# Kernel tuning notes

Measured on AMD Instinct MI355X. Metric: run time of the kernel, lower is better.

## Reference

```python
import jax, jax.numpy as jnp
import numpy as np

B, F = 2_000_000, 21
NUM_CLASSES = 7
RANGE_MIN, RANGE_MAX = 0.0, 1000.0  # normal_ranges[k] == (0, 1000) for all k


def setup_inputs() -> dict:
    key = jax.random.key(0)
    k1, k2, k3, k4 = jax.random.split(key, 4)
    inputs = jax.random.normal(k1, (B, F), dtype=jnp.float32) * 100.0
    # targets: integer sensor readings; column 2 must be a class value in {100,...,700}
    targets = jax.random.randint(k2, (B, F), -200, 1200, dtype=jnp.int32)
    cls_col = jax.random.randint(k3, (B,), 1, NUM_CLASSES + 1, dtype=jnp.int32) * 100
    targets = targets.at[:, 2].set(cls_col)
    weights = jax.random.uniform(k4, (NUM_CLASSES,), dtype=jnp.float32, minval=0.5, maxval=1.5)
    return {"inputs": inputs, "targets": targets, "weights": weights}


def reference(inputs, targets, weights):
    # class_to_index {100:0,...,700:6} == value // 100 - 1 (pure arithmetic, no host lookup)
    mapped = targets[:, 2] // 100 - 1                      # [B] int
    sample_w = weights[mapped]                              # [B]
    diff = inputs - targets.astype(inputs.dtype)            # [B, F]
    weighted_loss = jnp.mean(sample_w[:, None] * diff * diff, axis=1)  # [B]
    # range penalty on sensor value targets[:, 1] vs normal range (0, 1000)
    v = targets[:, 1].astype(inputs.dtype)                  # [B]
    below = jnp.square(v - RANGE_MIN)
    above = jnp.square(v - RANGE_MAX)
    pen = jnp.where(v < RANGE_MIN, below, jnp.where(v > RANGE_MAX, above, 0.0))
    penalty = jnp.sum(pen)                                  # scalar
    return jnp.mean(weighted_loss + penalty)
```

## Files before the change

kernel.cpp:

```cpp
#include <hip/hip_runtime.h>


#define TOTAL_ELEMS 42000000
#define NVEC (TOTAL_ELEMS / 4)
#define NBLK 2048
#define NTHR 256

__device__ __forceinline__ void accum4(int v, const float* __restrict__ x,
                                       const int* __restrict__ t, const float* ws,
                                       float& amain, float& apen)
{
    const int idx0 = v << 2;
    const float4 xf = reinterpret_cast<const float4*>(x)[v];
    const int4   ti = reinterpret_cast<const int4*>(t)[v];
    const int rowA = idx0 / 21;
    const int colA = idx0 - rowA * 21;
    const int rowB = (idx0 + 3) / 21;
    const float wA = ws[t[rowA * 21 + 2] / 100 - 1];
    const float wB = ws[t[rowB * 21 + 2] / 100 - 1];
    const float xs[4] = {xf.x, xf.y, xf.z, xf.w};
    const int   tv[4] = {ti.x, ti.y, ti.z, ti.w};
    #pragma unroll
    for (int j = 0; j < 4; ++j) {
        const int col   = colA + j;
        const float wj  = (col < 21) ? wA : wB;
        const int  ccol = (col < 21) ? col : col - 21;
        const float tf  = (float)tv[j];
        const float d   = xs[j] - tf;
        amain = fmaf(wj * d, d, amain);
        if (ccol == 1) {
            apen += tf < 0.f ? tf * tf
                  : (tf > 1000.f ? (tf - 1000.f) * (tf - 1000.f) : 0.f);
        }
    }
}

__global__ __launch_bounds__(NTHR) void wmse_main(
    const float* __restrict__ x, const int* __restrict__ t,
    const float* __restrict__ w, float* __restrict__ part)
{
    __shared__ float ws[8];
    if (threadIdx.x < 7) ws[threadIdx.x] = w[threadIdx.x];
    __syncthreads();

    float am0 = 0.f, am1 = 0.f, ap0 = 0.f, ap1 = 0.f;
    const int stride = NBLK * NTHR;
    for (int v = blockIdx.x * NTHR + threadIdx.x; v < NVEC; v += 2 * stride) {
        accum4(v, x, t, ws, am0, ap0);
        if (v + stride < NVEC) accum4(v + stride, x, t, ws, am1, ap1);
    }
    float amain = am0 + am1, apen = ap0 + ap1;

    #pragma unroll
    for (int off = 32; off > 0; off >>= 1) {
        amain += __shfl_down(amain, off);
        apen  += __shfl_down(apen,  off);
    }
    __shared__ float rm[4], rp[4];
    const int wid = threadIdx.x >> 6;
    if ((threadIdx.x & 63) == 0) { rm[wid] = amain; rp[wid] = apen; }
    __syncthreads();
    if (threadIdx.x == 0) {
        part[2 * blockIdx.x]     = rm[0] + rm[1] + rm[2] + rm[3];
        part[2 * blockIdx.x + 1] = rp[0] + rp[1] + rp[2] + rp[3];
    }
}

__global__ __launch_bounds__(256) void wmse_reduce(
    const float* __restrict__ part, float* __restrict__ out)
{
    float m = 0.f, p = 0.f;
    for (int i = threadIdx.x; i < NBLK; i += 256) {
        m += part[2 * i];
        p += part[2 * i + 1];
    }
    #pragma unroll
    for (int off = 32; off > 0; off >>= 1) {
        m += __shfl_down(m, off);
        p += __shfl_down(p, off);
    }
    __shared__ float rm[4], rp[4];
    const int wid = threadIdx.x >> 6;
    if ((threadIdx.x & 63) == 0) { rm[wid] = m; rp[wid] = p; }
    __syncthreads();
    if (threadIdx.x == 0) {
        out[0] = (rm[0] + rm[1] + rm[2] + rm[3]) * (1.0f / 42000000.0f)
               + (rp[0] + rp[1] + rp[2] + rp[3]);
    }
}

extern "C" void kernel_launch(void* const* d_in, const int* in_sizes, int n_in,
                              void* d_out, int out_size, void* d_ws, size_t ws_size,
                              hipStream_t stream)
{
    const float* x = (const float*)d_in[0];
    const int*   t = (const int*)d_in[1];
    const float* w = (const float*)d_in[2];
    float* part = (float*)d_ws;
    wmse_main<<<NBLK, NTHR, 0, stream>>>(x, t, w, part);
    wmse_reduce<<<1, 256, 0, stream>>>(part, (float*)d_out);
}
```

Baseline: 339.4 us.

## Software-pipeline loads with double-buffered chunk registers and branchless per-vector compute

Splits each float4/int4 chunk into a load phase and a compute phase, then runs a fully scheduled loop that keeps eight chunks in flight across two register buffers so memory latency overlaps arithmetic. It also halves the grid to 1024 blocks with a fixed trip count and replaces the per-element branchy weight and penalty logic with branchless selects and a clamp. The cost is higher register pressure and hardcoded sizing that only fits this exact element count (40*T plus a tail).

```diff
diff --git a/kernel.cpp b/kernel.cpp
--- a/kernel.cpp
+++ b/kernel.cpp
@@ -1,41 +1,48 @@
 #include <hip/hip_runtime.h>
 
 
-#define TOTAL_ELEMS 42000000
-#define NVEC (TOTAL_ELEMS / 4)
-#define NBLK 2048
+#define NVEC 10500000
+#define NBLK 1024
 #define NTHR 256
+#define T    (NBLK * NTHR)
 
-__device__ __forceinline__ void accum4(int v, const float* __restrict__ x,
-                                       const int* __restrict__ t, const float* ws,
-                                       float& amain, float& apen)
+struct CH { float4 xf; int4 ti; int tcA, tcB, colA; };
+
+__device__ __forceinline__ void ch_load(int v, const float* __restrict__ x,
+                                        const int* __restrict__ t, CH& c)
 {
     const int idx0 = v << 2;
-    const float4 xf = reinterpret_cast<const float4*>(x)[v];
-    const int4   ti = reinterpret_cast<const int4*>(t)[v];
+    c.xf = reinterpret_cast<const float4*>(x)[v];
+    c.ti = reinterpret_cast<const int4*>(t)[v];
     const int rowA = idx0 / 21;
-    const int colA = idx0 - rowA * 21;
+    c.colA = idx0 - rowA * 21;
     const int rowB = (idx0 + 3) / 21;
-    const float wA = ws[t[rowA * 21 + 2] / 100 - 1];
-    const float wB = ws[t[rowB * 21 + 2] / 100 - 1];
-    const float xs[4] = {xf.x, xf.y, xf.z, xf.w};
-    const int   tv[4] = {ti.x, ti.y, ti.z, ti.w};
-    #pragma unroll
-    for (int j = 0; j < 4; ++j) {
-        const int col   = colA + j;
-        const float wj  = (col < 21) ? wA : wB;
-        const int  ccol = (col < 21) ? col : col - 21;
-        const float tf  = (float)tv[j];
-        const float d   = xs[j] - tf;
-        amain = fmaf(wj * d, d, amain);
-        if (ccol == 1) {
-            apen += tf < 0.f ? tf * tf
-                  : (tf > 1000.f ? (tf - 1000.f) * (tf - 1000.f) : 0.f);
-        }
-    }
+    c.tcA = t[rowA * 21 + 2];
+    c.tcB = t[rowB * 21 + 2];
 }
 
-__global__ __launch_bounds__(NTHR) void wmse_main(
+__device__ __forceinline__ void ch_compute(const CH& c, const float* ws,
+                                           float& am, float& ap)
+{
+    const float wA = ws[c.tcA / 100 - 1];
+    const float wB = ws[c.tcB / 100 - 1];
+    const float tf0 = (float)c.ti.x, tf1 = (float)c.ti.y,
+                tf2 = (float)c.ti.z, tf3 = (float)c.ti.w;
+    const float d0 = c.xf.x - tf0, d1 = c.xf.y - tf1,
+                d2 = c.xf.z - tf2, d3 = c.xf.w - tf3;
+    const float q0 = d0 * d0, q1 = d1 * d1, q2 = d2 * d2, q3 = d3 * d3;
+    const int k = 21 - c.colA;
+    const float sB = ((1 >= k) ? q1 : 0.f) + ((2 >= k) ? q2 : 0.f)
+                   + ((3 >= k) ? q3 : 0.f);
+    const float sAll = (q0 + q1) + (q2 + q3);
+    am = fmaf(wA, sAll - sB, fmaf(wB, sB, am));
+    const int jp = (c.colA <= 1) ? (1 - c.colA) : (22 - c.colA);
+    const float pv = (jp == 0) ? tf0 : (jp == 1) ? tf1 : (jp == 2) ? tf2 : tf3;
+    const float r  = pv - fminf(fmaxf(pv, 0.f), 1000.f);
+    ap += (jp <= 3) ? r * r : 0.f;
+}
+
+__global__ __launch_bounds__(NTHR, 4) void wmse_main(
     const float* __restrict__ x, const int* __restrict__ t,
     const float* __restrict__ w, float* __restrict__ part)
 {
@@ -43,14 +50,38 @@
     if (threadIdx.x < 7) ws[threadIdx.x] = w[threadIdx.x];
     __syncthreads();
 
-    float am0 = 0.f, am1 = 0.f, ap0 = 0.f, ap1 = 0.f;
-    const int stride = NBLK * NTHR;
-    for (int v = blockIdx.x * NTHR + threadIdx.x; v < NVEC; v += 2 * stride) {
-        accum4(v, x, t, ws, am0, ap0);
-        if (v + stride < NVEC) accum4(v + stride, x, t, ws, am1, ap1);
+    const int tid = blockIdx.x * NTHR + threadIdx.x;
+    float amA = 0.f, apA = 0.f, amB = 0.f, apB = 0.f;
+    CH a0, a1, a2, a3, b0, b1, b2, b3;
+
+    ch_load(tid,         x, t, a0);
+    ch_load(tid + T,     x, t, a1);
+    ch_load(tid + 2 * T, x, t, a2);
+    ch_load(tid + 3 * T, x, t, a3);
+
+    int vs = tid;
+    #pragma unroll 1
+    for (int s = 0; s < 5; ++s) {
+        ch_load(vs + 4 * T, x, t, b0);
+        ch_load(vs + 5 * T, x, t, b1);
+        ch_load(vs + 6 * T, x, t, b2);
+        ch_load(vs + 7 * T, x, t, b3);
+        ch_compute(a0, ws, amA, apA); ch_compute(a1, ws, amA, apA);
+        ch_compute(a2, ws, amA, apA); ch_compute(a3, ws, amA, apA);
+        if (s < 4) {
+            ch_load(vs + 8 * T,  x, t, a0);
+            ch_load(vs + 9 * T,  x, t, a1);
+            ch_load(vs + 10 * T, x, t, a2);
+            ch_load(vs + 11 * T, x, t, a3);
+        }
+        ch_compute(b0, ws, amB, apB); ch_compute(b1, ws, amB, apB);
+        ch_compute(b2, ws, amB, apB); ch_compute(b3, ws, amB, apB);
+        vs += 8 * T;
     }
-    float amain = am0 + am1, apen = ap0 + ap1;
+    const int vt = tid + 40 * T;
+    if (vt < NVEC) { CH ct; ch_load(vt, x, t, ct); ch_compute(ct, ws, amA, apA); }
 
+    float amain = amA + amB, apen = apA + apB;
     #pragma unroll
     for (int off = 32; off > 0; off >>= 1) {
         amain += __shfl_down(amain, off);
```

New measurement: 357.1 us. 5.2% more time.
